# Performance work log

Hardware: AMD Instinct MI355X
Metric: run time of the kernel (lower is better)

Reference implementation:

```python
import jax, jax.numpy as jnp
import numpy as np

N_NODES = 20000
N_EDGES = 640000
NODE_NF = 256
EDGE_NF = 128
OUT_NF = 256


def setup_inputs() -> dict:
    key = jax.random.key(0)
    k1, k2, k3, k4, k5, k6, k7 = jax.random.split(key, 7)
    node_feats = jax.random.normal(k1, (N_NODES, NODE_NF), dtype=jnp.float32)
    edge_index = jax.random.randint(k2, (2, N_EDGES), 0, N_NODES, dtype=jnp.int64)
    edge_attr = jax.random.normal(k3, (N_EDGES, EDGE_NF), dtype=jnp.float32)
    # Learned params (match nn.Linear: y = x @ W.T + b). Store as [in, out] for clean einsum.
    s_e = 1.0 / np.sqrt(EDGE_NF)
    s_n = 1.0 / np.sqrt(NODE_NF)
    W_ij = jax.random.uniform(k4, (EDGE_NF, OUT_NF), jnp.float32, -s_e, s_e)
    b_ij = jax.random.uniform(k5, (OUT_NF,), jnp.float32, -s_e, s_e)
    W_i = jax.random.uniform(k6, (NODE_NF, OUT_NF), jnp.float32, -s_n, s_n)
    W_j = jax.random.uniform(k7, (NODE_NF, OUT_NF), jnp.float32, -s_n, s_n)
    return {
        "node_feats": node_feats,
        "edge_index": edge_index,
        "edge_attr": edge_attr,
        "W_ij": W_ij,
        "b_ij": b_ij,
        "W_i": W_i,
        "W_j": W_j,
    }


def reference(node_feats, edge_index, edge_attr, W_ij, b_ij, W_i, W_j):
    node_is = edge_index[0]
    node_js = edge_index[1]
    # Gather source/target node features per edge: [E, node_nf]
    f_i = node_feats[node_is] @ W_i  # [E, out_nf]
    f_j = node_feats[node_js] @ W_j  # [E, out_nf]
    f_ij = edge_attr @ W_ij + b_ij   # [E, out_nf]
    return jax.nn.relu(f_ij + f_i + f_j)
```

## Files before the change

kernel.cpp:

```cpp
#include <hip/hip_runtime.h>

#define N_NODES 20000
#define N_EDGES 640000
#define NODE_NF 256
#define EDGE_NF 128
#define OUT_NF  256

typedef short v8s __attribute__((ext_vector_type(8)));
typedef float v4f __attribute__((ext_vector_type(4)));

__device__ __forceinline__ float bf2f(unsigned short h) {
    unsigned int u = ((unsigned int)h) << 16;
    return __builtin_bit_cast(float, u);
}
__device__ __forceinline__ unsigned short f2bf(float f) {
    unsigned int u = __builtin_bit_cast(unsigned int, f);
    u = (u + 0x7FFFu + ((u >> 16) & 1u)) >> 16;
    return (unsigned short)u;
}
__device__ __forceinline__ v8s cvt8(v4f lo, v4f hi) {
    v8s r;
    #pragma unroll
    for (int j = 0; j < 4; ++j) {
        r[j]     = (short)f2bf(lo[j]);
        r[4 + j] = (short)f2bf(hi[j]);
    }
    return r;
}

__global__ __launch_bounds__(256) void node_proj_kernel(
    const float* __restrict__ node_feats,
    const float* __restrict__ W_i,
    const float* __restrict__ W_j,
    unsigned short* __restrict__ P_i,
    unsigned short* __restrict__ P_j)
{
    const int n0   = blockIdx.x * 16;
    const int wave = threadIdx.x >> 6;
    const int lane = threadIdx.x & 63;
    const int m    = lane & 15;
    const int quad = lane >> 4;

    const float*    W = (wave >= 2) ? W_j : W_i;
    unsigned short* P = (wave >= 2) ? P_j : P_i;
    const int colbase = (wave & 1) * 128;

    v4f acc[8];
    #pragma unroll
    for (int i = 0; i < 8; ++i) acc[i] = (v4f)(0.0f);

    for (int kt = 0; kt < 8; ++kt) {
        const int krow = kt * 32 + quad * 8;
        const float* arow = node_feats + (size_t)(n0 + m) * NODE_NF + krow;
        v8s afrag = cvt8(*reinterpret_cast<const v4f*>(arow),
                         *reinterpret_cast<const v4f*>(arow + 4));
        #pragma unroll
        for (int nt = 0; nt < 8; ++nt) {
            const int n = colbase + nt * 16 + m;
            v8s bfrag;
            #pragma unroll
            for (int j = 0; j < 8; ++j)
                bfrag[j] = (short)f2bf(W[(size_t)(krow + j) * OUT_NF + n]);
            acc[nt] = __builtin_amdgcn_mfma_f32_16x16x32_bf16(afrag, bfrag, acc[nt], 0, 0, 0);
        }
    }

    #pragma unroll
    for (int nt = 0; nt < 8; ++nt) {
        const int n = colbase + nt * 16 + m;
        #pragma unroll
        for (int r = 0; r < 4; ++r) {
            const int row = quad * 4 + r;
            P[(size_t)(n0 + row) * OUT_NF + n] = f2bf(acc[nt][r]);
        }
    }
}

__global__ __launch_bounds__(256) void edge_kernel(
    const float* __restrict__ edge_attr,
    const int*   __restrict__ edge_index,
    const float* __restrict__ W_ij,
    const float* __restrict__ bias,
    const unsigned short* __restrict__ P_i,
    const unsigned short* __restrict__ P_j,
    float*       __restrict__ out,
    int num_tiles)
{
    __shared__ float S[16][260];

    const int wave  = threadIdx.x >> 6;
    const int lane  = threadIdx.x & 63;
    const int m     = lane & 15;
    const int quad  = lane >> 4;
    const int wcol0 = wave * 64;

    v8s wf[4][4];
    #pragma unroll
    for (int kt = 0; kt < 4; ++kt) {
        const int krow = kt * 32 + quad * 8;
        #pragma unroll
        for (int nt = 0; nt < 4; ++nt) {
            const int n = wcol0 + nt * 16 + m;
            #pragma unroll
            for (int j = 0; j < 8; ++j)
                wf[kt][nt][j] = (short)f2bf(W_ij[(size_t)(krow + j) * OUT_NF + n]);
        }
    }

    const int s_edge = threadIdx.x & 15;
    const int s_c0   = (threadIdx.x >> 4) * 16;

    for (int tile = blockIdx.x; tile < num_tiles; tile += gridDim.x) {
        const int e0 = tile * 16;

        {
            const int src = edge_index[e0 + s_edge];
            const int dst = edge_index[N_EDGES + e0 + s_edge];
            const unsigned short* pi = P_i + (size_t)src * OUT_NF + s_c0;
            const unsigned short* pj = P_j + (size_t)dst * OUT_NF + s_c0;
            const float* bp = bias + s_c0;
            v8s pi0 = *reinterpret_cast<const v8s*>(pi);
            v8s pi1 = *reinterpret_cast<const v8s*>(pi + 8);
            v8s pj0 = *reinterpret_cast<const v8s*>(pj);
            v8s pj1 = *reinterpret_cast<const v8s*>(pj + 8);
            v4f b0 = *reinterpret_cast<const v4f*>(bp);
            v4f b1 = *reinterpret_cast<const v4f*>(bp + 4);
            v4f b2 = *reinterpret_cast<const v4f*>(bp + 8);
            v4f b3 = *reinterpret_cast<const v4f*>(bp + 12);
            #pragma unroll
            for (int c = 0; c < 4; ++c) {
                S[s_edge][s_c0 + c]      = bf2f((unsigned short)pi0[c])     + bf2f((unsigned short)pj0[c])     + b0[c];
                S[s_edge][s_c0 + 4 + c]  = bf2f((unsigned short)pi0[4 + c]) + bf2f((unsigned short)pj0[4 + c]) + b1[c];
                S[s_edge][s_c0 + 8 + c]  = bf2f((unsigned short)pi1[c])     + bf2f((unsigned short)pj1[c])     + b2[c];
                S[s_edge][s_c0 + 12 + c] = bf2f((unsigned short)pi1[4 + c]) + bf2f((unsigned short)pj1[4 + c]) + b3[c];
            }
        }
        __syncthreads();

        v4f acc[4];
        #pragma unroll
        for (int i = 0; i < 4; ++i) acc[i] = (v4f)(0.0f);
        #pragma unroll
        for (int kt = 0; kt < 4; ++kt) {
            const float* arow = edge_attr + (size_t)(e0 + m) * EDGE_NF + kt * 32 + quad * 8;
            v8s afrag = cvt8(*reinterpret_cast<const v4f*>(arow),
                             *reinterpret_cast<const v4f*>(arow + 4));
            #pragma unroll
            for (int nt = 0; nt < 4; ++nt)
                acc[nt] = __builtin_amdgcn_mfma_f32_16x16x32_bf16(afrag, wf[kt][nt], acc[nt], 0, 0, 0);
        }

        #pragma unroll
        for (int nt = 0; nt < 4; ++nt) {
            const int col = wcol0 + nt * 16 + m;
            #pragma unroll
            for (int r = 0; r < 4; ++r) {
                const int row = quad * 4 + r;
                float v = acc[nt][r] + S[row][col];
                v = v > 0.0f ? v : 0.0f;
                out[(size_t)(e0 + row) * OUT_NF + col] = v;
            }
        }
        __syncthreads();
    }
}

extern "C" void kernel_launch(void* const* d_in, const int* in_sizes, int n_in,
                              void* d_out, int out_size, void* d_ws, size_t ws_size,
                              hipStream_t stream) {
    const float* node_feats = (const float*)d_in[0];
    const int*   edge_index = (const int*)d_in[1];
    const float* edge_attr  = (const float*)d_in[2];
    const float* W_ij       = (const float*)d_in[3];
    const float* b_ij       = (const float*)d_in[4];
    const float* W_i        = (const float*)d_in[5];
    const float* W_j        = (const float*)d_in[6];
    float*       out        = (float*)d_out;

    unsigned short* P_i = (unsigned short*)d_ws;
    unsigned short* P_j = P_i + (size_t)N_NODES * OUT_NF;

    node_proj_kernel<<<N_NODES / 16, 256, 0, stream>>>(node_feats, W_i, W_j, P_i, P_j);
    edge_kernel<<<2560, 256, 0, stream>>>(edge_attr, edge_index, W_ij, b_ij,
                                          P_i, P_j, out, N_EDGES / 16);
}
```

Measured before the change: 1.172 ms.

## Software-pipeline edge gather with double-buffered LDS and index prefetch

Restructures the edge loop into a multi-stage software pipeline. Edge indices are prefetched three tiles ahead and P_i/P_j rows two tiles ahead, and the shared-memory sum buffer is double-buffered so the next tile's gathered sums are written while the current tile's MFMA and epilogue run. Edge_attr loads are issued early, bias is hoisted into registers, and one barrier per tile is removed. The aim is to hide gather latency behind compute, at the cost of more registers and LDS, which may lower occupancy.

```diff
diff --git a/kernel.cpp b/kernel.cpp
--- a/kernel.cpp
+++ b/kernel.cpp
@@ -86,7 +86,7 @@
     float*       __restrict__ out,
     int num_tiles)
 {
-    __shared__ float S[16][260];
+    __shared__ float S[2][16][260];
 
     const int wave  = threadIdx.x >> 6;
     const int lane  = threadIdx.x & 63;
@@ -110,41 +110,91 @@
     const int s_edge = threadIdx.x & 15;
     const int s_c0   = (threadIdx.x >> 4) * 16;
 
-    for (int tile = blockIdx.x; tile < num_tiles; tile += gridDim.x) {
-        const int e0 = tile * 16;
-
-        {
-            const int src = edge_index[e0 + s_edge];
-            const int dst = edge_index[N_EDGES + e0 + s_edge];
-            const unsigned short* pi = P_i + (size_t)src * OUT_NF + s_c0;
-            const unsigned short* pj = P_j + (size_t)dst * OUT_NF + s_c0;
-            const float* bp = bias + s_c0;
-            v8s pi0 = *reinterpret_cast<const v8s*>(pi);
-            v8s pi1 = *reinterpret_cast<const v8s*>(pi + 8);
-            v8s pj0 = *reinterpret_cast<const v8s*>(pj);
-            v8s pj1 = *reinterpret_cast<const v8s*>(pj + 8);
-            v4f b0 = *reinterpret_cast<const v4f*>(bp);
-            v4f b1 = *reinterpret_cast<const v4f*>(bp + 4);
-            v4f b2 = *reinterpret_cast<const v4f*>(bp + 8);
-            v4f b3 = *reinterpret_cast<const v4f*>(bp + 12);
-            #pragma unroll
-            for (int c = 0; c < 4; ++c) {
-                S[s_edge][s_c0 + c]      = bf2f((unsigned short)pi0[c])     + bf2f((unsigned short)pj0[c])     + b0[c];
-                S[s_edge][s_c0 + 4 + c]  = bf2f((unsigned short)pi0[4 + c]) + bf2f((unsigned short)pj0[4 + c]) + b1[c];
-                S[s_edge][s_c0 + 8 + c]  = bf2f((unsigned short)pi1[c])     + bf2f((unsigned short)pj1[c])     + b2[c];
-                S[s_edge][s_c0 + 12 + c] = bf2f((unsigned short)pi1[4 + c]) + bf2f((unsigned short)pj1[4 + c]) + b3[c];
-            }
-        }
-        __syncthreads();
-
-        v4f acc[4];
-        #pragma unroll
-        for (int i = 0; i < 4; ++i) acc[i] = (v4f)(0.0f);
+    v4f brg[4];
+    #pragma unroll
+    for (int i = 0; i < 4; ++i)
+        brg[i] = *reinterpret_cast<const v4f*>(bias + s_c0 + 4 * i);
+
+    const int stride = gridDim.x;
+    const int tile0  = blockIdx.x;
+    if (tile0 >= num_tiles) return;
+
+    int tB = tile0 + stride;     if (tB >= num_tiles) tB = tile0;
+    int tC = tile0 + 2 * stride; if (tC >= num_tiles) tC = tile0;
+    int tD = tile0 + 3 * stride; if (tD >= num_tiles) tD = tile0;
+
+    int srcA = edge_index[tile0 * 16 + s_edge];
+    int dstA = edge_index[N_EDGES + tile0 * 16 + s_edge];
+    int srcB = edge_index[tB * 16 + s_edge];
+    int dstB = edge_index[N_EDGES + tB * 16 + s_edge];
+    int srcC = edge_index[tC * 16 + s_edge];
+    int dstC = edge_index[N_EDGES + tC * 16 + s_edge];
+
+    v8s pi0, pi1, pj0, pj1;
+    {
+        const unsigned short* pp = P_i + (size_t)srcA * OUT_NF + s_c0;
+        const unsigned short* qq = P_j + (size_t)dstA * OUT_NF + s_c0;
+        pi0 = *reinterpret_cast<const v8s*>(pp);
+        pi1 = *reinterpret_cast<const v8s*>(pp + 8);
+        pj0 = *reinterpret_cast<const v8s*>(qq);
+        pj1 = *reinterpret_cast<const v8s*>(qq + 8);
+    }
+    #pragma unroll
+    for (int c = 0; c < 4; ++c) {
+        S[0][s_edge][s_c0 + c]      = bf2f((unsigned short)pi0[c])     + bf2f((unsigned short)pj0[c])     + brg[0][c];
+        S[0][s_edge][s_c0 + 4 + c]  = bf2f((unsigned short)pi0[4 + c]) + bf2f((unsigned short)pj0[4 + c]) + brg[1][c];
+        S[0][s_edge][s_c0 + 8 + c]  = bf2f((unsigned short)pi1[c])     + bf2f((unsigned short)pj1[c])     + brg[2][c];
+        S[0][s_edge][s_c0 + 12 + c] = bf2f((unsigned short)pi1[4 + c]) + bf2f((unsigned short)pj1[4 + c]) + brg[3][c];
+    }
+    {
+        const unsigned short* pp = P_i + (size_t)srcB * OUT_NF + s_c0;
+        const unsigned short* qq = P_j + (size_t)dstB * OUT_NF + s_c0;
+        pi0 = *reinterpret_cast<const v8s*>(pp);
+        pi1 = *reinterpret_cast<const v8s*>(pp + 8);
+        pj0 = *reinterpret_cast<const v8s*>(qq);
+        pj1 = *reinterpret_cast<const v8s*>(qq + 8);
+    }
+    __syncthreads();
+
+    int i = 0;
+    for (int t = tile0; t < num_tiles; t += stride, ++i) {
+        const int p  = i & 1;
+        const int e0 = t * 16;
+
+        int srcD = edge_index[tD * 16 + s_edge];
+        int dstD = edge_index[N_EDGES + tD * 16 + s_edge];
+
+        v4f ea[4][2];
         #pragma unroll
         for (int kt = 0; kt < 4; ++kt) {
             const float* arow = edge_attr + (size_t)(e0 + m) * EDGE_NF + kt * 32 + quad * 8;
-            v8s afrag = cvt8(*reinterpret_cast<const v4f*>(arow),
-                             *reinterpret_cast<const v4f*>(arow + 4));
+            ea[kt][0] = *reinterpret_cast<const v4f*>(arow);
+            ea[kt][1] = *reinterpret_cast<const v4f*>(arow + 4);
+        }
+
+        #pragma unroll
+        for (int c = 0; c < 4; ++c) {
+            S[p ^ 1][s_edge][s_c0 + c]      = bf2f((unsigned short)pi0[c])     + bf2f((unsigned short)pj0[c])     + brg[0][c];
+            S[p ^ 1][s_edge][s_c0 + 4 + c]  = bf2f((unsigned short)pi0[4 + c]) + bf2f((unsigned short)pj0[4 + c]) + brg[1][c];
+            S[p ^ 1][s_edge][s_c0 + 8 + c]  = bf2f((unsigned short)pi1[c])     + bf2f((unsigned short)pj1[c])     + brg[2][c];
+            S[p ^ 1][s_edge][s_c0 + 12 + c] = bf2f((unsigned short)pi1[4 + c]) + bf2f((unsigned short)pj1[4 + c]) + brg[3][c];
+        }
+
+        {
+            const unsigned short* pp = P_i + (size_t)srcC * OUT_NF + s_c0;
+            const unsigned short* qq = P_j + (size_t)dstC * OUT_NF + s_c0;
+            pi0 = *reinterpret_cast<const v8s*>(pp);
+            pi1 = *reinterpret_cast<const v8s*>(pp + 8);
+            pj0 = *reinterpret_cast<const v8s*>(qq);
+            pj1 = *reinterpret_cast<const v8s*>(qq + 8);
+        }
+
+        v4f acc[4];
+        #pragma unroll
+        for (int k = 0; k < 4; ++k) acc[k] = (v4f)(0.0f);
+        #pragma unroll
+        for (int kt = 0; kt < 4; ++kt) {
+            v8s afrag = cvt8(ea[kt][0], ea[kt][1]);
             #pragma unroll
             for (int nt = 0; nt < 4; ++nt)
                 acc[nt] = __builtin_amdgcn_mfma_f32_16x16x32_bf16(afrag, wf[kt][nt], acc[nt], 0, 0, 0);
@@ -156,12 +206,16 @@
             #pragma unroll
             for (int r = 0; r < 4; ++r) {
                 const int row = quad * 4 + r;
-                float v = acc[nt][r] + S[row][col];
+                float v = acc[nt][r] + S[p][row][col];
                 v = v > 0.0f ? v : 0.0f;
                 out[(size_t)(e0 + row) * OUT_NF + col] = v;
             }
         }
+
         __syncthreads();
+
+        srcC = srcD; dstC = dstD;
+        tD += stride; if (tD >= num_tiles) tD = tile0;
     }
 }
 
```

New measurement: 1.169 ms. About the same (-0.2%).

## Permute P layout to gather node projections directly into MFMA registers

Applied to the files above, without the earlier changes.

The node projection output is stored with a column permutation, so each lane's four MFMA output columns sit contiguously. The edge kernel can then gather them with one 8-byte load per row straight into registers, which removes the shared-memory staging buffer and both block barriers. Edge_attr loads are issued before the gathers so their latency overlaps, outputs use nontemporal stores, and the grid shrinks to 1024 blocks with launch_bounds occupancy 4. It relies on the matching column permutation in both kernels and adds register pressure.

```diff
diff --git a/kernel.cpp b/kernel.cpp
--- a/kernel.cpp
+++ b/kernel.cpp
@@ -7,6 +7,7 @@
 #define OUT_NF  256
 
 typedef short v8s __attribute__((ext_vector_type(8)));
+typedef short v4s __attribute__((ext_vector_type(4)));
 typedef float v4f __attribute__((ext_vector_type(4)));
 
 __device__ __forceinline__ float bf2f(unsigned short h) {
@@ -66,17 +67,21 @@
     }
 
     #pragma unroll
-    for (int nt = 0; nt < 8; ++nt) {
-        const int n = colbase + nt * 16 + m;
+    for (int r = 0; r < 4; ++r) {
+        const int row = quad * 4 + r;
+        v4s lo, hi;
         #pragma unroll
-        for (int r = 0; r < 4; ++r) {
-            const int row = quad * 4 + r;
-            P[(size_t)(n0 + row) * OUT_NF + n] = f2bf(acc[nt][r]);
+        for (int nt = 0; nt < 4; ++nt) {
+            lo[nt] = (short)f2bf(acc[nt][r]);
+            hi[nt] = (short)f2bf(acc[nt + 4][r]);
         }
+        unsigned short* base = P + (size_t)(n0 + row) * OUT_NF + colbase + m * 4;
+        *reinterpret_cast<v4s*>(base)      = lo;
+        *reinterpret_cast<v4s*>(base + 64) = hi;
     }
 }
 
-__global__ __launch_bounds__(256) void edge_kernel(
+__global__ __launch_bounds__(256, 4) void edge_kernel(
     const float* __restrict__ edge_attr,
     const int*   __restrict__ edge_index,
     const float* __restrict__ W_ij,
@@ -86,8 +91,6 @@
     float*       __restrict__ out,
     int num_tiles)
 {
-    __shared__ float S[16][260];
-
     const int wave  = threadIdx.x >> 6;
     const int lane  = threadIdx.x & 63;
     const int m     = lane & 15;
@@ -107,61 +110,57 @@
         }
     }
 
-    const int s_edge = threadIdx.x & 15;
-    const int s_c0   = (threadIdx.x >> 4) * 16;
+    float bv[4];
+    #pragma unroll
+    for (int nt = 0; nt < 4; ++nt)
+        bv[nt] = bias[wcol0 + nt * 16 + m];
 
-    for (int tile = blockIdx.x; tile < num_tiles; tile += gridDim.x) {
-        const int e0 = tile * 16;
+    for (int t = blockIdx.x; t < num_tiles; t += gridDim.x) {
+        const int e0 = t * 16;
 
-        {
-            const int src = edge_index[e0 + s_edge];
-            const int dst = edge_index[N_EDGES + e0 + s_edge];
-            const unsigned short* pi = P_i + (size_t)src * OUT_NF + s_c0;
-            const unsigned short* pj = P_j + (size_t)dst * OUT_NF + s_c0;
-            const float* bp = bias + s_c0;
-            v8s pi0 = *reinterpret_cast<const v8s*>(pi);
-            v8s pi1 = *reinterpret_cast<const v8s*>(pi + 8);
-            v8s pj0 = *reinterpret_cast<const v8s*>(pj);
-            v8s pj1 = *reinterpret_cast<const v8s*>(pj + 8);
-            v4f b0 = *reinterpret_cast<const v4f*>(bp);
-            v4f b1 = *reinterpret_cast<const v4f*>(bp + 4);
-            v4f b2 = *reinterpret_cast<const v4f*>(bp + 8);
-            v4f b3 = *reinterpret_cast<const v4f*>(bp + 12);
-            #pragma unroll
-            for (int c = 0; c < 4; ++c) {
-                S[s_edge][s_c0 + c]      = bf2f((unsigned short)pi0[c])     + bf2f((unsigned short)pj0[c])     + b0[c];
-                S[s_edge][s_c0 + 4 + c]  = bf2f((unsigned short)pi0[4 + c]) + bf2f((unsigned short)pj0[4 + c]) + b1[c];
-                S[s_edge][s_c0 + 8 + c]  = bf2f((unsigned short)pi1[c])     + bf2f((unsigned short)pj1[c])     + b2[c];
-                S[s_edge][s_c0 + 12 + c] = bf2f((unsigned short)pi1[4 + c]) + bf2f((unsigned short)pj1[4 + c]) + b3[c];
-            }
+        v4f ea[4][2];
+        #pragma unroll
+        for (int kt = 0; kt < 4; ++kt) {
+            const float* arow = edge_attr + (size_t)(e0 + m) * EDGE_NF + kt * 32 + quad * 8;
+            ea[kt][0] = *reinterpret_cast<const v4f*>(arow);
+            ea[kt][1] = *reinterpret_cast<const v4f*>(arow + 4);
         }
-        __syncthreads();
+
+        v4s pi4[4], pj4[4];
+        #pragma unroll
+        for (int r = 0; r < 4; ++r) {
+            const int e  = e0 + quad * 4 + r;
+            const int s  = edge_index[e];
+            const int d  = edge_index[N_EDGES + e];
+            pi4[r] = *reinterpret_cast<const v4s*>(P_i + (size_t)s * OUT_NF + wcol0 + m * 4);
+            pj4[r] = *reinterpret_cast<const v4s*>(P_j + (size_t)d * OUT_NF + wcol0 + m * 4);
+        }
 
         v4f acc[4];
         #pragma unroll
-        for (int i = 0; i < 4; ++i) acc[i] = (v4f)(0.0f);
+        for (int k = 0; k < 4; ++k) acc[k] = (v4f)(0.0f);
         #pragma unroll
         for (int kt = 0; kt < 4; ++kt) {
-            const float* arow = edge_attr + (size_t)(e0 + m) * EDGE_NF + kt * 32 + quad * 8;
-            v8s afrag = cvt8(*reinterpret_cast<const v4f*>(arow),
-                             *reinterpret_cast<const v4f*>(arow + 4));
+            v8s afrag = cvt8(ea[kt][0], ea[kt][1]);
             #pragma unroll
             for (int nt = 0; nt < 4; ++nt)
                 acc[nt] = __builtin_amdgcn_mfma_f32_16x16x32_bf16(afrag, wf[kt][nt], acc[nt], 0, 0, 0);
         }
 
         #pragma unroll
-        for (int nt = 0; nt < 4; ++nt) {
-            const int col = wcol0 + nt * 16 + m;
+        for (int r = 0; r < 4; ++r) {
+            const int row = quad * 4 + r;
+            float* orow = out + (size_t)(e0 + row) * OUT_NF + wcol0 + m;
             #pragma unroll
-            for (int r = 0; r < 4; ++r) {
-                const int row = quad * 4 + r;
-                float v = acc[nt][r] + S[row][col];
+            for (int nt = 0; nt < 4; ++nt) {
+                float v = acc[nt][r]
+                        + bf2f((unsigned short)pi4[r][nt])
+                        + bf2f((unsigned short)pj4[r][nt])
+                        + bv[nt];
                 v = v > 0.0f ? v : 0.0f;
-                out[(size_t)(e0 + row) * OUT_NF + col] = v;
+                __builtin_nontemporal_store(v, orow + nt * 16);
             }
         }
-        __syncthreads();
     }
 }
 
@@ -181,6 +180,6 @@
     unsigned short* P_j = P_i + (size_t)N_NODES * OUT_NF;
 
     node_proj_kernel<<<N_NODES / 16, 256, 0, stream>>>(node_feats, W_i, W_j, P_i, P_j);
-    edge_kernel<<<2560, 256, 0, stream>>>(edge_attr, edge_index, W_ij, b_ij,
+    edge_kernel<<<1024, 256, 0, stream>>>(edge_attr, edge_index, W_ij, b_ij,
                                           P_i, P_j, out, N_EDGES / 16);
 }
```

Result: faster. 1.106 ms (-5.6%).
